# Optimization experiments

Measured on AMD Instinct MI355X. Metric: run time of the kernel, lower is better.

## Reference

```python
import jax, jax.numpy as jnp
import numpy as np

THRESHOLD = 0.5
MARGIN = 0.5
MIN_PIXELS = 64


def make_grid(h, w):
    # Faithful to SpatialClustering.make_grid
    if w >= h:
        xm = jnp.broadcast_to(jnp.linspace(0.0, w / h, w).reshape(1, 1, w), (1, h, w))
        ym = jnp.broadcast_to(jnp.linspace(0.0, 1.0, h).reshape(1, h, 1), (1, h, w))
    else:
        xm = jnp.broadcast_to(jnp.linspace(0.0, 1.0, w).reshape(1, 1, w), (1, h, w))
        ym = jnp.broadcast_to(jnp.linspace(0.0, h / w, h).reshape(1, h, 1), (1, h, w))
    return jnp.concatenate([xm, ym], axis=0)  # (2, h, w)


def cluster_per_image(x, grid_flat):
    # x: (5, h, w); grid_flat: (2, N)
    c, h, w = x.shape
    N = h * w
    offset = x[0:2].reshape(2, N)
    sigma = x[2:4].reshape(2, N)
    seed_raw = x[4].reshape(N)

    spa_emb = jnp.tanh(offset) + grid_flat          # (2, N)
    seed_map = jax.nn.sigmoid(seed_raw)             # (N,)
    valid = seed_raw > THRESHOLD                    # (N,) == torch `mask`

    # In torch: masked_select restricts to `valid` pixels; here we keep the
    # full N-length arrays and carry `valid`/`unclustered` boolean masks.
    # unclustered starts as `valid`, so the torch outer guard
    # (mask.sum() > min_pixels) coincides with the first while-cond check.

    def cond(state):
        unclustered, inst, count, done = state
        return (jnp.sum(unclustered) > MIN_PIXELS) & jnp.logical_not(done)

    def body(state):
        unclustered, inst, count, done = state
        score = jnp.where(unclustered, seed_map, 0.0)
        idx = jnp.argmax(score)
        sc = score[idx]
        new_done = sc < THRESHOLD  # torch `break` -> revert this iteration's updates

        uncl2 = unclustered.at[idx].set(False)  # torch: unclustered[seed] = 0 before ratio
        center = spa_emb[:, idx]                # (2,)
        s = sigma[:, idx]                       # (2,)
        # exp(-sum((e-c)^2 / (2 s^2)))
        dist = jnp.exp(-jnp.sum((spa_emb - center[:, None]) ** 2 / (2.0 * s[:, None] ** 2), axis=0))  # (N,)
        proposal = (dist > MARGIN) & valid

        pc = jnp.sum(proposal)
        uc = jnp.sum(proposal & uncl2)
        # torch: proposal.sum() > min_pixels  and  unclustered[proposal].sum()/proposal.sum() > 0.5
        accept = (pc > MIN_PIXELS) & (2 * uc > pc)

        inst_new = jnp.where(accept & proposal, count, inst)
        count_new = count + accept.astype(jnp.int32)
        uncl_new = uncl2 & jnp.logical_not(proposal)  # torch: unclustered[proposal] = 0

        unclustered = jnp.where(new_done, unclustered, uncl_new)
        inst = jnp.where(new_done, inst, inst_new)
        count = jnp.where(new_done, count, count_new)
        return (unclustered, inst, count, new_done)

    init = (valid, jnp.zeros(N, dtype=jnp.int32), jnp.int32(1), jnp.array(False))
    _, inst, _, _ = jax.lax.while_loop(cond, body, init)
    return inst.reshape(h, w)


def setup_inputs() -> dict:
    key = jax.random.key(0)
    k1, k2, k3 = jax.random.split(key, 3)
    B, H, W = 4, 512, 1024
    offset = jax.random.normal(k1, (B, 2, H, W), dtype=jnp.float32)
    # sigma in [0.2, 0.45]: realistic per-pixel bandwidths so exp-distance
    # proposals cover cluster-sized regions and the greedy loop terminates.
    sigma = jax.random.uniform(k2, (B, 2, H, W), dtype=jnp.float32, minval=0.2, maxval=0.45)
    seed = jax.random.normal(k3, (B, 1, H, W), dtype=jnp.float32)
    tag_pred = jnp.concatenate([offset, sigma, seed], axis=1)  # (B, 5, H, W)
    return {"tag_pred": tag_pred}


def reference(tag_pred):
    b, c, h, w = tag_pred.shape
    grid_flat = make_grid(h, w).reshape(2, h * w)
    f = lambda x: cluster_per_image(x, grid_flat)
    inst = jax.lax.map(f, tag_pred)  # sequential per-image greedy clustering
    return inst.astype(jnp.uint8)    # (b, h, w) instance map, ids 0 = background
```

## Files before the change

kernel.cpp:

```cpp
#include <hip/hip_runtime.h>
#include <math.h>

#define BATCH 4
#define HH 512
#define WW 1024
#define NPIX (HH*WW)
#define CCAP 196608
#define GX 64
#define GY 48
#define NCELL (GX*GY)
#define CELL 0.0625f
#define INVCELL 16.0f
#define SEGSZ 512
#define NSEGMAX (CCAP/SEGSZ)
#define DLCAP 2048
#define CKCAP 800
#define CKBCAP 512

__device__ __forceinline__ float xla_tanhf(float x) {
  if (fabsf(x) < 0.0004f) return x;
  float xc = fminf(fmaxf(x, -7.90531110763549805f), 7.90531110763549805f);
  float x2 = __fmul_rn(xc, xc);
  float p = -2.76076847742355e-16f;
  p = fmaf(x2, p, 2.00018790482477e-13f);
  p = fmaf(x2, p, -8.60467152213735e-11f);
  p = fmaf(x2, p, 5.12229709037114e-08f);
  p = fmaf(x2, p, 1.48572235717979e-05f);
  p = fmaf(x2, p, 6.37261928875436e-04f);
  p = fmaf(x2, p, 4.89352455891786e-03f);
  p = __fmul_rn(xc, p);
  float q = fmaf(x2, 1.19825839466702e-06f, 1.18534705686654e-04f);
  q = fmaf(x2, q, 2.26843463243900e-03f);
  q = fmaf(x2, q, 4.89352518554385e-03f);
  return __fdiv_rn(p, q);
}

__device__ __forceinline__ float xla_expf(float x) {
  float xc = fminf(fmaxf(x, -87.3365478515625f), 88.72283935546875f);
  float m = floorf(fmaf(xc, 1.44269504088896341f, 0.5f));
  float r = fmaf(m, -0.693359375f, xc);
  r = fmaf(m, 2.12194440e-4f, r);
  float r2 = __fmul_rn(r, r);
  float p = 1.9875691500e-4f;
  p = fmaf(p, r, 1.3981999507e-3f);
  p = fmaf(p, r, 8.3334519073e-3f);
  p = fmaf(p, r, 4.1665795894e-2f);
  p = fmaf(p, r, 1.6666665459e-1f);
  p = fmaf(p, r, 5.0000001201e-1f);
  float y = fmaf(r2, p, r);
  y = __fadd_rn(y, 1.0f);
  return ldexpf(y, (int)m);
}

__device__ __forceinline__ float xla_sigmoidf(float x) {
  return fmaf(0.5f, xla_tanhf(__fmul_rn(0.5f, x)), 0.5f);
}

__device__ __forceinline__ bool prop_test(float2 e, float cx, float cy,
                                          float den0, float den1,
                                          float inv0, float inv1) {
  float d0 = __fsub_rn(e.x, cx), d1 = __fsub_rn(e.y, cy);
  float dd0 = __fmul_rn(d0, d0), dd1 = __fmul_rn(d1, d1);
  float zf = fmaf(dd0, inv0, __fmul_rn(dd1, inv1));
  if (zf < 0.6921472f) return true;
  if (zf <= 0.6941472f) {
    float t0 = __fdiv_rn(dd0, den0);
    float t1 = __fdiv_rn(dd1, den1);
    float z = __fadd_rn(t0, t1);
    return xla_expf(-z) > 0.5f;
  }
  return false;
}

__device__ __forceinline__ int cell_of_x(float ex) {
  int c = (int)((ex + 1.0f) * INVCELL);
  return min(max(c, 0), GX - 1);
}
__device__ __forceinline__ int cell_of_y(float ey) {
  int c = (int)((ey + 1.0f) * INVCELL);
  return min(max(c, 0), GY - 1);
}

__device__ __forceinline__ unsigned wave_max_bcast_u32(unsigned x) {
  unsigned t;
  t = (unsigned)__builtin_amdgcn_update_dpp(0, (int)x, 0x111, 0xf, 0xf, false); if (t > x) x = t;
  t = (unsigned)__builtin_amdgcn_update_dpp(0, (int)x, 0x112, 0xf, 0xf, false); if (t > x) x = t;
  t = (unsigned)__builtin_amdgcn_update_dpp(0, (int)x, 0x114, 0xf, 0xf, false); if (t > x) x = t;
  t = (unsigned)__builtin_amdgcn_update_dpp(0, (int)x, 0x118, 0xf, 0xf, false); if (t > x) x = t;
  t = (unsigned)__builtin_amdgcn_update_dpp(0, (int)x, 0x142, 0xa, 0xf, false); if (t > x) x = t;
  t = (unsigned)__builtin_amdgcn_update_dpp(0, (int)x, 0x143, 0xc, 0xf, false); if (t > x) x = t;
  return (unsigned)__builtin_amdgcn_readlane((int)x, 63);
}

__device__ __forceinline__ int wave_sum_bcast_i32(int x) {
  x += __builtin_amdgcn_update_dpp(0, x, 0x111, 0xf, 0xf, false);
  x += __builtin_amdgcn_update_dpp(0, x, 0x112, 0xf, 0xf, false);
  x += __builtin_amdgcn_update_dpp(0, x, 0x114, 0xf, 0xf, false);
  x += __builtin_amdgcn_update_dpp(0, x, 0x118, 0xf, 0xf, false);
  x += __builtin_amdgcn_update_dpp(0, x, 0x142, 0xa, 0xf, false);
  x += __builtin_amdgcn_update_dpp(0, x, 0x143, 0xc, 0xf, false);
  return __builtin_amdgcn_readlane(x, 63);
}

__device__ __forceinline__ int wave_scan_incl_i32(int x) {
  x += __builtin_amdgcn_update_dpp(0, x, 0x111, 0xf, 0xf, false);
  x += __builtin_amdgcn_update_dpp(0, x, 0x112, 0xf, 0xf, false);
  x += __builtin_amdgcn_update_dpp(0, x, 0x114, 0xf, 0xf, false);
  x += __builtin_amdgcn_update_dpp(0, x, 0x118, 0xf, 0xf, false);
  x += __builtin_amdgcn_update_dpp(0, x, 0x142, 0xa, 0xf, false);
  x += __builtin_amdgcn_update_dpp(0, x, 0x143, 0xc, 0xf, false);
  return x;
}


__global__ __launch_bounds__(1024) void fill_kernel(int* out, int val, int n) {
  int i = blockIdx.x * 1024 + threadIdx.x;
  if (i < n) out[i] = val;
}

__global__ __launch_bounds__(1024) void hist_kernel(const float* __restrict__ in,
                                                    int* __restrict__ out,
                                                    int* __restrict__ hist) {
  __shared__ int lh[NCELL];
  int tid = threadIdx.x;
  int gid = blockIdx.x * 1024 + tid;
  int b = gid >> 19;
  int p = gid & (NPIX - 1);
  for (int j = tid; j < NCELL; j += 1024) lh[j] = 0;
  __syncthreads();
  const float* base = in + (size_t)b * 5 * NPIX;
  float seed = base[(size_t)4 * NPIX + p];
  out[gid] = 0;
  if (seed > 0.5f) {
    float ox = base[p];
    float oy = base[(size_t)NPIX + p];
    int col = p & (WW - 1);
    int row = p >> 10;
    float gx = __fmul_rn((float)col, 2.0f / 1023.0f);
    float gy = __fmul_rn((float)row, 1.0f / 511.0f);
    float ex = __fadd_rn(xla_tanhf(ox), gx);
    float ey = __fadd_rn(xla_tanhf(oy), gy);
    atomicAdd(&lh[cell_of_y(ey) * GX + cell_of_x(ex)], 1);
  }
  __syncthreads();
  for (int j = tid; j < NCELL; j += 1024) {
    int c = lh[j];
    if (c) atomicAdd(&hist[b * NCELL + j], c);
  }
}

__global__ __launch_bounds__(1024) void scan_kernel(const int* __restrict__ hist,
                                                    int* __restrict__ off,
                                                    int* __restrict__ cursor) {
  __shared__ int s_c[NCELL];
  __shared__ int s_ps[1024];
  int b = blockIdx.x, t = threadIdx.x;
  const int* h = hist + b * NCELL;
  for (int i = t; i < NCELL; i += 1024) s_c[i] = h[i];
  __syncthreads();
  int a = s_c[3 * t], b2 = s_c[3 * t + 1], c2 = s_c[3 * t + 2];
  int th = a + b2 + c2;
  s_ps[t] = th;
  __syncthreads();
  for (int d = 1; d < 1024; d <<= 1) {
    int v = (t >= d) ? s_ps[t - d] : 0;
    __syncthreads();
    s_ps[t] += v;
    __syncthreads();
  }
  int excl = s_ps[t] - th;
  int* ob = off + b * (NCELL + 1);
  int* cb = cursor + b * NCELL;
  ob[3 * t] = excl;              cb[3 * t] = excl;
  ob[3 * t + 1] = excl + a;      cb[3 * t + 1] = excl + a;
  ob[3 * t + 2] = excl + a + b2; cb[3 * t + 2] = excl + a + b2;
  if (t == 1023) ob[NCELL] = s_ps[1023];
}

__global__ __launch_bounds__(1024) void scatter_kernel(const float* __restrict__ in,
                                                       int* __restrict__ cursor,
                                                       float2* __restrict__ emb,
                                                       int2* __restrict__ pk) {
  __shared__ int lh[NCELL];
  __shared__ int lbase[NCELL];
  int tid = threadIdx.x;
  int gid = blockIdx.x * 1024 + tid;
  int b = gid >> 19;
  int p = gid & (NPIX - 1);
  for (int j = tid; j < NCELL; j += 1024) lh[j] = 0;
  __syncthreads();
  const float* base = in + (size_t)b * 5 * NPIX;
  float seed = base[(size_t)4 * NPIX + p];
  bool valid = seed > 0.5f;
  float ex = 0.0f, ey = 0.0f, smv = 0.0f;
  int cell = 0, sl = 0;
  if (valid) {
    float ox = base[p];
    float oy = base[(size_t)NPIX + p];
    int col = p & (WW - 1);
    int row = p >> 10;
    float gx = __fmul_rn((float)col, 2.0f / 1023.0f);
    float gy = __fmul_rn((float)row, 1.0f / 511.0f);
    ex = __fadd_rn(xla_tanhf(ox), gx);
    ey = __fadd_rn(xla_tanhf(oy), gy);
    smv = xla_sigmoidf(seed);
    cell = cell_of_y(ey) * GX + cell_of_x(ex);
    sl = atomicAdd(&lh[cell], 1);
  }
  __syncthreads();
  for (int j = tid; j < NCELL; j += 1024) {
    int c = lh[j];
    if (c) lbase[j] = atomicAdd(&cursor[b * NCELL + j], c);
  }
  __syncthreads();
  if (valid) {
    int slot = lbase[cell] + sl;
    if (slot < CCAP) {
      emb[(size_t)b * CCAP + slot] = make_float2(ex, ey);
      pk[(size_t)b * CCAP + slot]  = make_int2(__float_as_int(smv), p);
    }
  }
}

__device__ __forceinline__ void seg_rescan(int s, int V, int lane,
    const unsigned* s_uncl, const int2* __restrict__ pk,
    const float2* __restrict__ emb, const float* __restrict__ base,
    unsigned long long* s_segkey, int* s_segci, float4* s_segaux,
    float4* s_segaux2, bool checkAlive) {
  unsigned long long bk = 0ULL; int bci = -1; int bpx = 0;
  #pragma unroll
  for (int j = 0; j < 8; ++j) {
    int i = (s << 9) + (j << 6) + lane;
    if (i < V) {
      bool alive = !checkAlive || ((s_uncl[i >> 5] >> (i & 31)) & 1u);
      if (alive) {
        int2 v = pk[i];
        unsigned long long k = ((unsigned long long)(unsigned)v.x << 32) | (unsigned)(~v.y);
        if (k > bk) { bk = k; bci = i; bpx = v.y; }
      }
    }
  }
  unsigned bs = (unsigned)(bk >> 32);
  unsigned ms = wave_max_bcast_u32(bs);
  if (ms == 0u) {
    if (lane == 0) { s_segkey[s] = 0ULL; s_segci[s] = -1; }
    return;
  }
  unsigned long long tie = __ballot(bs == ms);
  bool winner;
  if (__popcll(tie) == 1ULL) {
    winner = (bs == ms);
  } else {
    unsigned long long mk = bk;
    #pragma unroll
    for (int o = 1; o < 64; o <<= 1) {
      unsigned long long ok = __shfl_xor(mk, o);
      if (ok > mk) mk = ok;
    }
    winner = (bk == mk);
  }
  if (winner) {
    s_segkey[s] = bk; s_segci[s] = bci;
    float2 e = emb[bci];
    float sxv = base[(size_t)2 * NPIX + bpx];
    float syv = base[(size_t)3 * NPIX + bpx];
    float d0 = __fmul_rn(2.0f, __fmul_rn(sxv, sxv));
    float d1 = __fmul_rn(2.0f, __fmul_rn(syv, syv));
    s_segaux[s] = make_float4(e.x, e.y, d0, d1);
    float i0v = 1.0f / d0;
    float i1v = 1.0f / d1;
    float ryv = sqrtf(__fmul_rn(d1, 0.6971472f)) * 1.00001f;
    s_segaux2[s] = make_float4(i0v, i1v, ryv, 0.0f);
  }
}

__global__ __launch_bounds__(1024) void cluster_kernel(const float* __restrict__ in,
                                                       int* __restrict__ out,
                                                       const float2* __restrict__ emb_all,
                                                       const int2* __restrict__ pk_all,
                                                       const int* __restrict__ off_g) {
  __shared__ unsigned int s_uncl[CCAP / 32];
  __shared__ int s_off[NCELL + 1];
  __shared__ unsigned long long s_segkey[NSEGMAX];
  __shared__ int s_segci[NSEGMAX];
  __shared__ float4 s_segaux[NSEGMAX];
  __shared__ float4 s_segaux2[NSEGMAX];
  __shared__ int s_dlist[DLCAP];
  __shared__ unsigned long long s_ck[CKCAP];
  __shared__ ulonglong2 s_ckbA[CKBCAP];
  __shared__ ulonglong2 s_ckbB[CKBCAP];
  __shared__ int s_pc[2];
  __shared__ int s_uc[2];
  __shared__ int s_nd[2];

  int b = blockIdx.x;
  int tid = threadIdx.x;
  int lane = tid & 63;
  int wid = tid >> 6;
  const int* offb = off_g + b * (NCELL + 1);
  int V = offb[NCELL];
  const float2* emb = emb_all + (size_t)b * CCAP;
  const int2*   pk  = pk_all  + (size_t)b * CCAP;
  int* outb = out + (size_t)b * NPIX;
  const float* base = in + (size_t)b * 5 * NPIX;

  if (V > CCAP) {
    for (int i = tid; i < NPIX; i += 1024) outb[i] = 1000000;
    return;
  }
  int NSEG = (V + SEGSZ - 1) >> 9;
  int Vm1 = V - 1;

  for (int i = tid; i <= NCELL; i += 1024) s_off[i] = offb[i];
  for (int w = tid; w < CCAP / 32; w += 1024) {
    int basebit = w << 5;
    unsigned m;
    if (basebit + 32 <= V)      m = 0xffffffffu;
    else if (basebit >= V)      m = 0u;
    else                        m = (1u << (V - basebit)) - 1u;
    s_uncl[w] = m;
  }
  if (tid < 2) { s_pc[tid] = 0; s_uc[tid] = 0; s_nd[tid] = 0; }
  __syncthreads();

  for (int s = wid; s < NSEG; s += 16)
    seg_rescan(s, V, lane, s_uncl, pk, emb, base, s_segkey, s_segci, s_segaux,
               s_segaux2, false);
  __syncthreads();

  int ucount = V, count = 1, guard = 0;
  int t = 0;
  while (ucount > 64 && guard++ <= CCAP) {
    int cur = t & 1, nxt = cur ^ 1;

    unsigned long long lk = 0ULL; int lsg = -1;
    for (int s = lane; s < NSEG; s += 64) {
      unsigned long long v = s_segkey[s];
      if (v > lk) { lk = v; lsg = s; }
    }
    unsigned ls = (unsigned)(lk >> 32);
    unsigned gs = wave_max_bcast_u32(ls);
    if (gs == 0u) break;
    float sm = __uint_as_float(gs);
    if (sm < 0.5f) break;
    unsigned long long bmask = __ballot(ls == gs);
    int src, sg;
    if (__popcll(bmask) == 1ULL) {
      src = __builtin_ctzll(bmask);
      sg = __shfl(lsg, src);
    } else {
      unsigned long long gk = lk;
      #pragma unroll
      for (int o = 1; o < 64; o <<= 1) {
        unsigned long long ok = __shfl_xor(gk, o);
        if (ok > gk) gk = ok;
      }
      unsigned long long bm2 = __ballot(lk == gk);
      src = __builtin_ctzll(bm2);
      sg = __shfl(lsg, src);
    }

    float4 aux = s_segaux[sg];
    float4 ax2 = s_segaux2[sg];
    float cx = aux.x, cy = aux.y, den0 = aux.z, den1 = aux.w;
    float inv0 = ax2.x;
    float inv1 = ax2.y;
    float ry = ax2.z;
    int r0 = cell_of_y(cy - ry);
    int r1 = cell_of_y(cy + ry);
    int nr = r1 - r0 + 1;

    int ck = 0, rs_l = 0, re_l = 0, m0_l = 0, m1_l = 0, startl = 0;
    if (lane < nr) {
      int r = r0 + lane;
      float ylo = fmaf((float)r, CELL, -1.0f);
      float dy = fmaxf(0.0f, fmaxf(ylo - cy, cy - (ylo + CELL))) * 0.999999f;
      float rem = 0.6971472f - dy * dy * inv1;
      if (rem > 0.0f) {
        float dxm = sqrtf(den0 * rem) * 1.00001f;
        int c0 = cell_of_x(cx - dxm), c1 = cell_of_x(cx + dxm);
        int rbase = r * GX;
        rs_l = s_off[rbase + c0]; re_l = s_off[rbase + c1 + 1];
        m0_l = rs_l; m1_l = rs_l;
        float dyc = fmaxf(fabsf(ylo - cy), fabsf(ylo + CELL - cy)) + 1e-5f;
        float remI = 0.6920f - dyc * dyc * inv1;
        if (remI > 0.0f) {
          float dxin = sqrtf(den0 * remI) * 0.9999f;
          int a  = (int)ceilf(fmaf(cx - dxin, INVCELL, INVCELL) + 1e-3f);
          int bb = (int)floorf(fmaf(cx + dxin, INVCELL, INVCELL) - 1e-3f) - 1;
          a = max(a, c0); bb = min(bb, c1);
          if (a <= bb) { m0_l = s_off[rbase + a]; m1_l = s_off[rbase + bb + 1]; }
        }
        startl = rs_l & ~31;
        ck = (re_l > rs_l) ? ((re_l - startl + 255) >> 8) : 0;
      }
    }
    int cum = wave_scan_incl_i32(ck);
    int nc = __builtin_amdgcn_readlane(cum, 63);
    int excl = cum - ck;
    if (lane < nr && ck) {
      for (int k = 0; k < ck; ++k) {
        int i0k = startl + (k << 8);
        int ssk = max(rs_l - i0k, 0);
        int lok = min(max(m0_l - i0k, 0), 256);
        int h2k = min(max(m1_l - i0k, 0), 256);
        int enk = min(re_l - i0k, 256);
        s_ck[excl + k] = (unsigned long long)(unsigned)(i0k >> 5)
                       | ((unsigned long long)(unsigned)ssk << 13)
                       | ((unsigned long long)(unsigned)lok << 19)
                       | ((unsigned long long)(unsigned)h2k << 28)
                       | ((unsigned long long)(unsigned)enk << 37);
      }
    }

    int pc = 0, uc = 0;
    int c = wid;
    unsigned long long ed = (c < nc) ? s_ck[c] : 0ULL;
    while (c < nc) {
      int cn = c + 16;
      unsigned long long epre = (cn < nc) ? s_ck[cn] : 0ULL;
      int i0 = ((int)(ed & 0x1fff)) << 5;
      int ss = (int)((ed >> 13) & 0x3f);
      int lo = (int)((ed >> 19) & 0x1ff);
      int h2 = (int)((ed >> 28) & 0x1ff);
      int en = (int)((ed >> 37) & 0x1ff);
      int idx1 = lane + 64, idx2 = lane + 128, idx3 = lane + 192;
      bool p0, p1, p2, p3;
      if (lo <= ss && h2 >= en) {
        p0 = lane >= ss && lane < en;
        p1 = idx1 < en; p2 = idx2 < en; p3 = idx3 < en;
      } else {
        int ia = min(i0 + lane, Vm1),  ib = min(i0 + idx1, Vm1);
        int ic = min(i0 + idx2, Vm1),  id = min(i0 + idx3, Vm1);
        float2 e0 = emb[ia], e1 = emb[ib], e2 = emb[ic], e3 = emb[id];
        bool t0 = prop_test(e0, cx, cy, den0, den1, inv0, inv1);
        bool t1 = prop_test(e1, cx, cy, den0, den1, inv0, inv1);
        bool t2 = prop_test(e2, cx, cy, den0, den1, inv0, inv1);
        bool t3 = prop_test(e3, cx, cy, den0, den1, inv0, inv1);
        p0 = (lane >= ss && lane < en) && ((lane >= lo && lane < h2) || t0);
        p1 = (idx1 < en) && ((idx1 >= lo && idx1 < h2) || t1);
        p2 = (idx2 < en) && ((idx2 >= lo && idx2 < h2) || t2);
        p3 = (idx3 < en) && ((idx3 >= lo && idx3 < h2) || t3);
      }
      unsigned long long bm0 = __ballot(p0);
      unsigned long long bm1 = __ballot(p1);
      unsigned long long bm2 = __ballot(p2);
      unsigned long long bm3 = __ballot(p3);
      if (c < CKBCAP) {
        if (lane == 0)      { ulonglong2 v; v.x = bm0; v.y = bm1; s_ckbA[c] = v; }
        else if (lane == 1) { ulonglong2 v; v.x = bm2; v.y = bm3; s_ckbB[c] = v; }
      }
      if ((bm0 | bm1 | bm2 | bm3) != 0ULL && lane < 8) {
        unsigned long long bsel = (lane < 2) ? bm0 : (lane < 4) ? bm1
                                 : (lane < 6) ? bm2 : bm3;
        unsigned bits = (unsigned)(bsel >> ((lane & 1) << 5));
        pc += __popc(bits);
        if (bits) {
          unsigned tw = (unsigned)(i0 >> 5) + (unsigned)lane;
          unsigned old = atomicAnd(&s_uncl[tw], ~bits);
          unsigned remv = old & bits;
          if (remv) {
            uc += __popc(remv);
            int seg = (int)(tw >> 4);
            int ciw = s_segci[seg];
            if ((ciw >> 5) == (int)tw && ((remv >> (ciw & 31)) & 1u)) {
              int pos = atomicAdd(&s_nd[cur], 1);
              if (pos < DLCAP) s_dlist[pos] = seg;
            }
          }
        }
      }
      c = cn; ed = epre;
    }
    int pcW = wave_sum_bcast_i32(pc);
    int ucW = wave_sum_bcast_i32(uc);
    if (lane == 0 && (pcW | ucW)) {
      if (pcW) atomicAdd(&s_pc[cur], pcW);
      if (ucW) atomicAdd(&s_uc[cur], ucW);
    }
    __syncthreads();

    int pcT = s_pc[cur];
    int ucR = s_uc[cur];
    int ndRaw = s_nd[cur];
    bool accept = (pcT > 64) && (2 * (ucR - 1) > pcT);
    int label = count & 255;
    if (accept) count++;
    ucount -= ucR;
    if (tid == 0) { s_pc[nxt] = 0; s_uc[nxt] = 0; s_nd[nxt] = 0; }

    if (accept) {
      for (int c2 = wid; c2 < nc; c2 += 16) {
        unsigned long long e = s_ck[c2];
        int i0 = ((int)(e & 0x1fff)) << 5;
        if (c2 < CKBCAP) {
          ulonglong2 ba = s_ckbA[c2];
          ulonglong2 bb = s_ckbB[c2];
          if ((ba.x >> lane) & 1ULL) outb[pk[i0 + lane].y] = label;
          if ((ba.y >> lane) & 1ULL) outb[pk[i0 + 64 + lane].y] = label;
          if ((bb.x >> lane) & 1ULL) outb[pk[i0 + 128 + lane].y] = label;
          if ((bb.y >> lane) & 1ULL) outb[pk[i0 + 192 + lane].y] = label;
        } else {
          int ss = (int)((e >> 13) & 0x3f);
          int lo = (int)((e >> 19) & 0x1ff);
          int h2 = (int)((e >> 28) & 0x1ff);
          int en = (int)((e >> 37) & 0x1ff);
          #pragma unroll
          for (int g = 0; g < 4; ++g) {
            int idx = (g << 6) + lane;
            if (idx >= ss && idx < en &&
                ((idx >= lo && idx < h2) ||
                 prop_test(emb[i0 + idx], cx, cy, den0, den1, inv0, inv1)))
              outb[pk[i0 + idx].y] = label;
          }
        }
      }
    }

    if (ndRaw > DLCAP) {
      for (int s = wid; s < NSEG; s += 16)
        seg_rescan(s, V, lane, s_uncl, pk, emb, base, s_segkey, s_segci,
                   s_segaux, s_segaux2, true);
    } else {
      for (int d = wid; d < ndRaw; d += 16)
        seg_rescan(s_dlist[d], V, lane, s_uncl, pk, emb, base, s_segkey,
                   s_segci, s_segaux, s_segaux2, true);
    }
    __syncthreads();
    t++;
  }
}


extern "C" void kernel_launch(void* const* d_in, const int* in_sizes, int n_in,
                              void* d_out, int out_size, void* d_ws, size_t ws_size,
                              hipStream_t stream) {
  const float* in = (const float*)d_in[0];
  int* out = (int*)d_out;

  size_t hist_bytes = (size_t)BATCH * NCELL * sizeof(int);
  size_t off_bytes  = (size_t)BATCH * (NCELL + 1) * sizeof(int);
  size_t cur_bytes  = (size_t)BATCH * NCELL * sizeof(int);
  size_t emb_bytes  = (size_t)BATCH * CCAP * sizeof(float2);
  size_t pk_bytes   = (size_t)BATCH * CCAP * sizeof(int2);

  size_t o_hist = 256;
  size_t o_off  = (o_hist + hist_bytes + 255) & ~(size_t)255;
  size_t o_cur  = (o_off + off_bytes + 255) & ~(size_t)255;
  size_t o_emb  = (o_cur + cur_bytes + 255) & ~(size_t)255;
  size_t o_pk   = (o_emb + emb_bytes + 255) & ~(size_t)255;
  size_t need   = o_pk + pk_bytes;

  if (ws_size < need) {
    fill_kernel<<<(out_size + 1023) / 1024, 1024, 0, stream>>>(out, 2000000, out_size);
    return;
  }

  int*    hist = (int*)((char*)d_ws + o_hist);
  int*    off  = (int*)((char*)d_ws + o_off);
  int*    cur  = (int*)((char*)d_ws + o_cur);
  float2* emb  = (float2*)((char*)d_ws + o_emb);
  int2*   pk   = (int2*)((char*)d_ws + o_pk);

  hipMemsetAsync(hist, 0, hist_bytes, stream);
  hist_kernel<<<(BATCH * NPIX) / 1024, 1024, 0, stream>>>(in, out, hist);
  scan_kernel<<<BATCH, 1024, 0, stream>>>(hist, off, cur);
  scatter_kernel<<<(BATCH * NPIX) / 1024, 1024, 0, stream>>>(in, cur, emb, pk);
  cluster_kernel<<<BATCH, 1024, 0, stream>>>(in, out, emb, pk, off);
}
```

Measured before the change: 796.5 us.

## Process two non-overlapping seeds per greedy iteration with per-wave dynamic chunk scheduling

```diff
diff --git a/kernel.cpp b/kernel.cpp
--- a/kernel.cpp
+++ b/kernel.cpp
@@ -14,7 +14,8 @@
 #define SEGSZ 512
 #define NSEGMAX (CCAP/SEGSZ)
 #define DLCAP 2048
-#define CKCAP 800
+#define CKSEED 800
+#define CKCAP (2*CKSEED)
 #define CKBCAP 512
 
 __device__ __forceinline__ float xla_tanhf(float x) {
@@ -81,17 +82,6 @@
   return min(max(c, 0), GY - 1);
 }
 
-__device__ __forceinline__ unsigned wave_max_bcast_u32(unsigned x) {
-  unsigned t;
-  t = (unsigned)__builtin_amdgcn_update_dpp(0, (int)x, 0x111, 0xf, 0xf, false); if (t > x) x = t;
-  t = (unsigned)__builtin_amdgcn_update_dpp(0, (int)x, 0x112, 0xf, 0xf, false); if (t > x) x = t;
-  t = (unsigned)__builtin_amdgcn_update_dpp(0, (int)x, 0x114, 0xf, 0xf, false); if (t > x) x = t;
-  t = (unsigned)__builtin_amdgcn_update_dpp(0, (int)x, 0x118, 0xf, 0xf, false); if (t > x) x = t;
-  t = (unsigned)__builtin_amdgcn_update_dpp(0, (int)x, 0x142, 0xa, 0xf, false); if (t > x) x = t;
-  t = (unsigned)__builtin_amdgcn_update_dpp(0, (int)x, 0x143, 0xc, 0xf, false); if (t > x) x = t;
-  return (unsigned)__builtin_amdgcn_readlane((int)x, 63);
-}
-
 __device__ __forceinline__ int wave_sum_bcast_i32(int x) {
   x += __builtin_amdgcn_update_dpp(0, x, 0x111, 0xf, 0xf, false);
   x += __builtin_amdgcn_update_dpp(0, x, 0x112, 0xf, 0xf, false);
@@ -110,6 +100,18 @@
   x += __builtin_amdgcn_update_dpp(0, x, 0x142, 0xa, 0xf, false);
   x += __builtin_amdgcn_update_dpp(0, x, 0x143, 0xc, 0xf, false);
   return x;
+}
+
+__device__ __forceinline__ void wave_max_key64(unsigned &h, unsigned &l) {
+#define KSTEP(ctrl, rm)                                                        \
+  { unsigned nh = (unsigned)__builtin_amdgcn_update_dpp(0, (int)h, ctrl, rm, 0xf, false); \
+    unsigned nl = (unsigned)__builtin_amdgcn_update_dpp(0, (int)l, ctrl, rm, 0xf, false); \
+    if (nh > h || (nh == h && nl > l)) { h = nh; l = nl; } }
+  KSTEP(0x111, 0xf) KSTEP(0x112, 0xf) KSTEP(0x114, 0xf) KSTEP(0x118, 0xf)
+  KSTEP(0x142, 0xa) KSTEP(0x143, 0xc)
+#undef KSTEP
+  h = (unsigned)__builtin_amdgcn_readlane((int)h, 63);
+  l = (unsigned)__builtin_amdgcn_readlane((int)l, 63);
 }
 
 
@@ -225,9 +227,9 @@
 __device__ __forceinline__ void seg_rescan(int s, int V, int lane,
     const unsigned* s_uncl, const int2* __restrict__ pk,
     const float2* __restrict__ emb, const float* __restrict__ base,
-    unsigned long long* s_segkey, int* s_segci, float4* s_segaux,
-    float4* s_segaux2, bool checkAlive) {
-  unsigned long long bk = 0ULL; int bci = -1; int bpx = 0;
+    unsigned long long* s_segkey, unsigned long long* s_segkey2,
+    int* s_segci, float4* s_segaux, float4* s_segaux2, bool checkAlive) {
+  unsigned k1h = 0, k1l = 0, k2h = 0, k2l = 0; int ci1 = -1, bpx = 0;
   #pragma unroll
   for (int j = 0; j < 8; ++j) {
     int i = (s << 9) + (j << 6) + lane;
@@ -235,33 +237,30 @@
       bool alive = !checkAlive || ((s_uncl[i >> 5] >> (i & 31)) & 1u);
       if (alive) {
         int2 v = pk[i];
-        unsigned long long k = ((unsigned long long)(unsigned)v.x << 32) | (unsigned)(~v.y);
-        if (k > bk) { bk = k; bci = i; bpx = v.y; }
-      }
-    }
-  }
-  unsigned bs = (unsigned)(bk >> 32);
-  unsigned ms = wave_max_bcast_u32(bs);
-  if (ms == 0u) {
-    if (lane == 0) { s_segkey[s] = 0ULL; s_segci[s] = -1; }
+        unsigned vh = (unsigned)v.x, vl = (unsigned)(~v.y);
+        if (vh > k1h || (vh == k1h && vl > k1l)) {
+          k2h = k1h; k2l = k1l; k1h = vh; k1l = vl; ci1 = i; bpx = v.y;
+        } else if (vh > k2h || (vh == k2h && vl > k2l)) {
+          k2h = vh; k2l = vl;
+        }
+      }
+    }
+  }
+  unsigned m1h = k1h, m1l = k1l;
+  wave_max_key64(m1h, m1l);
+  if (m1h == 0u) {
+    if (lane == 0) { s_segkey[s] = 0ULL; s_segkey2[s] = 0ULL; s_segci[s] = -1; }
     return;
   }
-  unsigned long long tie = __ballot(bs == ms);
-  bool winner;
-  if (__popcll(tie) == 1ULL) {
-    winner = (bs == ms);
-  } else {
-    unsigned long long mk = bk;
-    #pragma unroll
-    for (int o = 1; o < 64; o <<= 1) {
-      unsigned long long ok = __shfl_xor(mk, o);
-      if (ok > mk) mk = ok;
-    }
-    winner = (bk == mk);
-  }
-  if (winner) {
-    s_segkey[s] = bk; s_segci[s] = bci;
-    float2 e = emb[bci];
+  bool own = (k1h == m1h && k1l == m1l);
+  unsigned ch = own ? k2h : k1h, cl = own ? k2l : k1l;
+  unsigned m2h = ch, m2l = cl;
+  wave_max_key64(m2h, m2l);
+  if (lane == 0) s_segkey2[s] = ((unsigned long long)m2h << 32) | m2l;
+  if (own) {
+    s_segkey[s] = ((unsigned long long)m1h << 32) | m1l;
+    s_segci[s] = ci1;
+    float2 e = emb[ci1];
     float sxv = base[(size_t)2 * NPIX + bpx];
     float syv = base[(size_t)3 * NPIX + bpx];
     float d0 = __fmul_rn(2.0f, __fmul_rn(sxv, sxv));
@@ -270,7 +269,8 @@
     float i0v = 1.0f / d0;
     float i1v = 1.0f / d1;
     float ryv = sqrtf(__fmul_rn(d1, 0.6971472f)) * 1.00001f;
-    s_segaux2[s] = make_float4(i0v, i1v, ryv, 0.0f);
+    float rxv = sqrtf(__fmul_rn(d0, 0.6971472f)) * 1.00001f;
+    s_segaux2[s] = make_float4(i0v, i1v, ryv, rxv);
   }
 }
 
@@ -282,16 +282,19 @@
   __shared__ unsigned int s_uncl[CCAP / 32];
   __shared__ int s_off[NCELL + 1];
   __shared__ unsigned long long s_segkey[NSEGMAX];
+  __shared__ unsigned long long s_segkey2[NSEGMAX];
   __shared__ int s_segci[NSEGMAX];
   __shared__ float4 s_segaux[NSEGMAX];
   __shared__ float4 s_segaux2[NSEGMAX];
   __shared__ int s_dlist[DLCAP];
   __shared__ unsigned long long s_ck[CKCAP];
-  __shared__ ulonglong2 s_ckbA[CKBCAP];
-  __shared__ ulonglong2 s_ckbB[CKBCAP];
-  __shared__ int s_pc[2];
-  __shared__ int s_uc[2];
+  __shared__ ulonglong2 s_ckbA[2 * CKBCAP];
+  __shared__ ulonglong2 s_ckbB[2 * CKBCAP];
+  __shared__ int s_pc4[4];
+  __shared__ int s_uc4[4];
+  __shared__ int s_ckpos4[4];
   __shared__ int s_nd[2];
+  __shared__ int s_ncq[2];
 
   int b = blockIdx.x;
   int tid = threadIdx.x;
@@ -320,12 +323,13 @@
     else                        m = (1u << (V - basebit)) - 1u;
     s_uncl[w] = m;
   }
-  if (tid < 2) { s_pc[tid] = 0; s_uc[tid] = 0; s_nd[tid] = 0; }
+  if (tid < 4) { s_pc4[tid] = 0; s_uc4[tid] = 0; s_ckpos4[tid] = 0; }
+  if (tid < 2) { s_nd[tid] = 0; }
   __syncthreads();
 
   for (int s = wid; s < NSEG; s += 16)
-    seg_rescan(s, V, lane, s_uncl, pk, emb, base, s_segkey, s_segci, s_segaux,
-               s_segaux2, false);
+    seg_rescan(s, V, lane, s_uncl, pk, emb, base, s_segkey, s_segkey2,
+               s_segci, s_segaux, s_segaux2, false);
   __syncthreads();
 
   int ucount = V, count = 1, guard = 0;
@@ -333,61 +337,80 @@
   while (ucount > 64 && guard++ <= CCAP) {
     int cur = t & 1, nxt = cur ^ 1;
 
-    unsigned long long lk = 0ULL; int lsg = -1;
+    unsigned a1h = 0, a1l = 0, a2h = 0, a2l = 0; int asg1 = -1, asg2 = -1;
     for (int s = lane; s < NSEG; s += 64) {
       unsigned long long v = s_segkey[s];
-      if (v > lk) { lk = v; lsg = s; }
-    }
-    unsigned ls = (unsigned)(lk >> 32);
-    unsigned gs = wave_max_bcast_u32(ls);
-    if (gs == 0u) break;
-    float sm = __uint_as_float(gs);
-    if (sm < 0.5f) break;
-    unsigned long long bmask = __ballot(ls == gs);
-    int src, sg;
-    if (__popcll(bmask) == 1ULL) {
-      src = __builtin_ctzll(bmask);
-      sg = __shfl(lsg, src);
-    } else {
-      unsigned long long gk = lk;
-      #pragma unroll
-      for (int o = 1; o < 64; o <<= 1) {
-        unsigned long long ok = __shfl_xor(gk, o);
-        if (ok > gk) gk = ok;
-      }
-      unsigned long long bm2 = __ballot(lk == gk);
-      src = __builtin_ctzll(bm2);
-      sg = __shfl(lsg, src);
-    }
-
-    float4 aux = s_segaux[sg];
-    float4 ax2 = s_segaux2[sg];
-    float cx = aux.x, cy = aux.y, den0 = aux.z, den1 = aux.w;
-    float inv0 = ax2.x;
-    float inv1 = ax2.y;
-    float ry = ax2.z;
-    int r0 = cell_of_y(cy - ry);
-    int r1 = cell_of_y(cy + ry);
+      unsigned vh = (unsigned)(v >> 32), vl = (unsigned)v;
+      if (vh > a1h || (vh == a1h && vl > a1l)) {
+        a2h = a1h; a2l = a1l; asg2 = asg1; a1h = vh; a1l = vl; asg1 = s;
+      } else if (vh > a2h || (vh == a2h && vl > a2l)) {
+        a2h = vh; a2l = vl; asg2 = s;
+      }
+    }
+    unsigned m1h = a1h, m1l = a1l;
+    wave_max_key64(m1h, m1l);
+    if (m1h == 0u) break;
+    if (__uint_as_float(m1h) < 0.5f) break;
+    bool own1 = (a1h == m1h && a1l == m1l);
+    int src1 = __builtin_ctzll(__ballot(own1));
+    int sg1 = __shfl(asg1, src1);
+    unsigned ch = own1 ? a2h : a1h, cl2 = own1 ? a2l : a1l;
+    int csg = own1 ? asg2 : asg1;
+    unsigned m2h = ch, m2l = cl2;
+    wave_max_key64(m2h, m2l);
+
+    float4 auxA = s_segaux[sg1];
+    float4 ax2A = s_segaux2[sg1];
+    int kk = 1, sg2 = -1;
+    float4 auxB = make_float4(0.f, 0.f, 1.f, 1.f);
+    float4 ax2B = make_float4(1.f, 1.f, 0.f, 0.f);
+    if (m2h != 0u) {
+      bool own2 = (ch == m2h && cl2 == m2l);
+      int src2 = __builtin_ctzll(__ballot(own2));
+      sg2 = __shfl(csg, src2);
+      unsigned long long k2s = s_segkey2[sg1];
+      unsigned kh = (unsigned)(k2s >> 32), kl = (unsigned)k2s;
+      bool hidden_bigger = (kh > m2h) || (kh == m2h && kl > m2l);
+      if (!hidden_bigger) {
+        auxB = s_segaux[sg2];
+        ax2B = s_segaux2[sg2];
+        bool ovl = (fabsf(auxA.x - auxB.x) <= (ax2A.w + ax2B.w)) &&
+                   (fabsf(auxA.y - auxB.y) <= (ax2A.z + ax2B.z));
+        if (!ovl) kk = 2;
+      }
+    }
+
+    int myseed = (kk == 2) ? (wid & 1) : 0;
+    float cxS = myseed ? auxB.x : auxA.x;
+    float cyS = myseed ? auxB.y : auxA.y;
+    float d0S = myseed ? auxB.z : auxA.z;
+    float d1S = myseed ? auxB.w : auxA.w;
+    float i0S = myseed ? ax2B.x : ax2A.x;
+    float i1S = myseed ? ax2B.y : ax2A.y;
+    float ryS = myseed ? ax2B.z : ax2A.z;
+    int qb = myseed * CKSEED;
+    int r0 = cell_of_y(cyS - ryS);
+    int r1 = cell_of_y(cyS + ryS);
     int nr = r1 - r0 + 1;
 
     int ck = 0, rs_l = 0, re_l = 0, m0_l = 0, m1_l = 0, startl = 0;
     if (lane < nr) {
       int r = r0 + lane;
       float ylo = fmaf((float)r, CELL, -1.0f);
-      float dy = fmaxf(0.0f, fmaxf(ylo - cy, cy - (ylo + CELL))) * 0.999999f;
-      float rem = 0.6971472f - dy * dy * inv1;
+      float dy = fmaxf(0.0f, fmaxf(ylo - cyS, cyS - (ylo + CELL))) * 0.999999f;
+      float rem = 0.6971472f - dy * dy * i1S;
       if (rem > 0.0f) {
-        float dxm = sqrtf(den0 * rem) * 1.00001f;
-        int c0 = cell_of_x(cx - dxm), c1 = cell_of_x(cx + dxm);
+        float dxm = sqrtf(d0S * rem) * 1.00001f;
+        int c0 = cell_of_x(cxS - dxm), c1 = cell_of_x(cxS + dxm);
         int rbase = r * GX;
         rs_l = s_off[rbase + c0]; re_l = s_off[rbase + c1 + 1];
         m0_l = rs_l; m1_l = rs_l;
-        float dyc = fmaxf(fabsf(ylo - cy), fabsf(ylo + CELL - cy)) + 1e-5f;
-        float remI = 0.6920f - dyc * dyc * inv1;
+        float dyc = fmaxf(fabsf(ylo - cyS), fabsf(ylo + CELL - cyS)) + 1e-5f;
+        float remI = 0.6920f - dyc * dyc * i1S;
         if (remI > 0.0f) {
-          float dxin = sqrtf(den0 * remI) * 0.9999f;
-          int a  = (int)ceilf(fmaf(cx - dxin, INVCELL, INVCELL) + 1e-3f);
-          int bb = (int)floorf(fmaf(cx + dxin, INVCELL, INVCELL) - 1e-3f) - 1;
+          float dxin = sqrtf(d0S * remI) * 0.9999f;
+          int a  = (int)ceilf(fmaf(cxS - dxin, INVCELL, INVCELL) + 1e-3f);
+          int bb = (int)floorf(fmaf(cxS + dxin, INVCELL, INVCELL) - 1e-3f) - 1;
           a = max(a, c0); bb = min(bb, c1);
           if (a <= bb) { m0_l = s_off[rbase + a]; m1_l = s_off[rbase + bb + 1]; }
         }
@@ -396,29 +419,35 @@
       }
     }
     int cum = wave_scan_incl_i32(ck);
-    int nc = __builtin_amdgcn_readlane(cum, 63);
+    int ncmine = __builtin_amdgcn_readlane(cum, 63);
     int excl = cum - ck;
+    if (ncmine > CKSEED) ncmine = CKSEED;
     if (lane < nr && ck) {
       for (int k = 0; k < ck; ++k) {
+        int q = excl + k;
+        if (q >= CKSEED) break;
         int i0k = startl + (k << 8);
         int ssk = max(rs_l - i0k, 0);
         int lok = min(max(m0_l - i0k, 0), 256);
         int h2k = min(max(m1_l - i0k, 0), 256);
         int enk = min(re_l - i0k, 256);
-        s_ck[excl + k] = (unsigned long long)(unsigned)(i0k >> 5)
-                       | ((unsigned long long)(unsigned)ssk << 13)
-                       | ((unsigned long long)(unsigned)lok << 19)
-                       | ((unsigned long long)(unsigned)h2k << 28)
-                       | ((unsigned long long)(unsigned)enk << 37);
-      }
-    }
+        s_ck[qb + q] = (unsigned long long)(unsigned)(i0k >> 5)
+                     | ((unsigned long long)(unsigned)ssk << 13)
+                     | ((unsigned long long)(unsigned)lok << 19)
+                     | ((unsigned long long)(unsigned)h2k << 28)
+                     | ((unsigned long long)(unsigned)enk << 37);
+      }
+    }
+    if (lane == 0) s_ncq[myseed] = ncmine;
 
     int pc = 0, uc = 0;
-    int c = wid;
-    unsigned long long ed = (c < nc) ? s_ck[c] : 0ULL;
-    while (c < nc) {
-      int cn = c + 16;
-      unsigned long long epre = (cn < nc) ? s_ck[cn] : 0ULL;
+    int* ckposp = &s_ckpos4[cur * 2 + myseed];
+    for (;;) {
+      int pos;
+      if (lane == 0) pos = atomicAdd(ckposp, 1);
+      pos = __shfl(pos, 0);
+      if (pos >= ncmine) break;
+      unsigned long long ed = s_ck[qb + pos];
       int i0 = ((int)(ed & 0x1fff)) << 5;
       int ss = (int)((ed >> 13) & 0x3f);
       int lo = (int)((ed >> 19) & 0x1ff);
@@ -433,10 +462,10 @@
         int ia = min(i0 + lane, Vm1),  ib = min(i0 + idx1, Vm1);
         int ic = min(i0 + idx2, Vm1),  id = min(i0 + idx3, Vm1);
         float2 e0 = emb[ia], e1 = emb[ib], e2 = emb[ic], e3 = emb[id];
-        bool t0 = prop_test(e0, cx, cy, den0, den1, inv0, inv1);
-        bool t1 = prop_test(e1, cx, cy, den0, den1, inv0, inv1);
-        bool t2 = prop_test(e2, cx, cy, den0, den1, inv0, inv1);
-        bool t3 = prop_test(e3, cx, cy, den0, den1, inv0, inv1);
+        bool t0 = prop_test(e0, cxS, cyS, d0S, d1S, i0S, i1S);
+        bool t1 = prop_test(e1, cxS, cyS, d0S, d1S, i0S, i1S);
+        bool t2 = prop_test(e2, cxS, cyS, d0S, d1S, i0S, i1S);
+        bool t3 = prop_test(e3, cxS, cyS, d0S, d1S, i0S, i1S);
         p0 = (lane >= ss && lane < en) && ((lane >= lo && lane < h2) || t0);
         p1 = (idx1 < en) && ((idx1 >= lo && idx1 < h2) || t1);
         p2 = (idx2 < en) && ((idx2 >= lo && idx2 < h2) || t2);
@@ -446,9 +475,10 @@
       unsigned long long bm1 = __ballot(p1);
       unsigned long long bm2 = __ballot(p2);
       unsigned long long bm3 = __ballot(p3);
-      if (c < CKBCAP) {
-        if (lane == 0)      { ulonglong2 v; v.x = bm0; v.y = bm1; s_ckbA[c] = v; }
-        else if (lane == 1) { ulonglong2 v; v.x = bm2; v.y = bm3; s_ckbB[c] = v; }
+      if (pos < CKBCAP) {
+        int bidx = (myseed << 9) + pos;
+        if (lane == 0)      { ulonglong2 v; v.x = bm0; v.y = bm1; s_ckbA[bidx] = v; }
+        else if (lane == 1) { ulonglong2 v; v.x = bm2; v.y = bm3; s_ckbB[bidx] = v; }
       }
       if ((bm0 | bm1 | bm2 | bm3) != 0ULL && lane < 8) {
         unsigned long long bsel = (lane < 2) ? bm0 : (lane < 4) ? bm1
@@ -464,42 +494,51 @@
             int seg = (int)(tw >> 4);
             int ciw = s_segci[seg];
             if ((ciw >> 5) == (int)tw && ((remv >> (ciw & 31)) & 1u)) {
-              int pos = atomicAdd(&s_nd[cur], 1);
-              if (pos < DLCAP) s_dlist[pos] = seg;
+              int dpos = atomicAdd(&s_nd[cur], 1);
+              if (dpos < DLCAP) s_dlist[dpos] = seg;
             }
           }
         }
       }
-      c = cn; ed = epre;
     }
     int pcW = wave_sum_bcast_i32(pc);
     int ucW = wave_sum_bcast_i32(uc);
     if (lane == 0 && (pcW | ucW)) {
-      if (pcW) atomicAdd(&s_pc[cur], pcW);
-      if (ucW) atomicAdd(&s_uc[cur], ucW);
+      if (pcW) atomicAdd(&s_pc4[cur * 2 + myseed], pcW);
+      if (ucW) atomicAdd(&s_uc4[cur * 2 + myseed], ucW);
     }
     __syncthreads();
 
-    int pcT = s_pc[cur];
-    int ucR = s_uc[cur];
+    int pcT0 = s_pc4[cur * 2 + 0], ucR0 = s_uc4[cur * 2 + 0];
+    int pcT1 = s_pc4[cur * 2 + 1], ucR1 = s_uc4[cur * 2 + 1];
     int ndRaw = s_nd[cur];
-    bool accept = (pcT > 64) && (2 * (ucR - 1) > pcT);
-    int label = count & 255;
-    if (accept) count++;
-    ucount -= ucR;
-    if (tid == 0) { s_pc[nxt] = 0; s_uc[nxt] = 0; s_nd[nxt] = 0; }
-
-    if (accept) {
-      for (int c2 = wid; c2 < nc; c2 += 16) {
+    int nc0 = s_ncq[0];
+    int nc1q = (kk == 2) ? s_ncq[1] : 0;
+    bool acc0 = (pcT0 > 64) && (2 * (ucR0 - 1) > pcT0);
+    bool valid1 = (kk == 2) && (ucount - ucR0 > 64);
+    bool acc1 = valid1 && (pcT1 > 64) && (2 * (ucR1 - 1) > pcT1);
+    int label0 = count & 255; if (acc0) count++;
+    int label1 = count & 255; if (acc1) count++;
+    ucount -= ucR0;
+    if (valid1) ucount -= ucR1;
+    if (tid == 0) {
+      s_pc4[nxt * 2] = 0; s_pc4[nxt * 2 + 1] = 0;
+      s_uc4[nxt * 2] = 0; s_uc4[nxt * 2 + 1] = 0;
+      s_nd[nxt] = 0;
+      s_ckpos4[nxt * 2] = 0; s_ckpos4[nxt * 2 + 1] = 0;
+    }
+
+    if (acc0) {
+      for (int c2 = wid; c2 < nc0; c2 += 16) {
         unsigned long long e = s_ck[c2];
         int i0 = ((int)(e & 0x1fff)) << 5;
         if (c2 < CKBCAP) {
           ulonglong2 ba = s_ckbA[c2];
           ulonglong2 bb = s_ckbB[c2];
-          if ((ba.x >> lane) & 1ULL) outb[pk[i0 + lane].y] = label;
-          if ((ba.y >> lane) & 1ULL) outb[pk[i0 + 64 + lane].y] = label;
-          if ((bb.x >> lane) & 1ULL) outb[pk[i0 + 128 + lane].y] = label;
-          if ((bb.y >> lane) & 1ULL) outb[pk[i0 + 192 + lane].y] = label;
+          if ((ba.x >> lane) & 1ULL) outb[pk[i0 + lane].y] = label0;
+          if ((ba.y >> lane) & 1ULL) outb[pk[i0 + 64 + lane].y] = label0;
+          if ((bb.x >> lane) & 1ULL) outb[pk[i0 + 128 + lane].y] = label0;
+          if ((bb.y >> lane) & 1ULL) outb[pk[i0 + 192 + lane].y] = label0;
         } else {
           int ss = (int)((e >> 13) & 0x3f);
           int lo = (int)((e >> 19) & 0x1ff);
@@ -510,21 +549,52 @@
             int idx = (g << 6) + lane;
             if (idx >= ss && idx < en &&
                 ((idx >= lo && idx < h2) ||
-                 prop_test(emb[i0 + idx], cx, cy, den0, den1, inv0, inv1)))
-              outb[pk[i0 + idx].y] = label;
+                 prop_test(emb[i0 + idx], auxA.x, auxA.y, auxA.z, auxA.w,
+                           ax2A.x, ax2A.y)))
+              outb[pk[i0 + idx].y] = label0;
           }
         }
       }
     }
+    if (acc1) {
+      for (int c2 = wid; c2 < nc1q; c2 += 16) {
+        unsigned long long e = s_ck[CKSEED + c2];
+        int i0 = ((int)(e & 0x1fff)) << 5;
+        if (c2 < CKBCAP) {
+          ulonglong2 ba = s_ckbA[CKBCAP + c2];
+          ulonglong2 bb = s_ckbB[CKBCAP + c2];
+          if ((ba.x >> lane) & 1ULL) outb[pk[i0 + lane].y] = label1;
+          if ((ba.y >> lane) & 1ULL) outb[pk[i0 + 64 + lane].y] = label1;
+          if ((bb.x >> lane) & 1ULL) outb[pk[i0 + 128 + lane].y] = label1;
+          if ((bb.y >> lane) & 1ULL) outb[pk[i0 + 192 + lane].y] = label1;
+        } else {
+          int ss = (int)((e >> 13) & 0x3f);
+          int lo = (int)((e >> 19) & 0x1ff);
+          int h2 = (int)((e >> 28) & 0x1ff);
+          int en = (int)((e >> 37) & 0x1ff);
+          #pragma unroll
+          for (int g = 0; g < 4; ++g) {
+            int idx = (g << 6) + lane;
+            if (idx >= ss && idx < en &&
+                ((idx >= lo && idx < h2) ||
+                 prop_test(emb[i0 + idx], auxB.x, auxB.y, auxB.z, auxB.w,
+                           ax2B.x, ax2B.y)))
+              outb[pk[i0 + idx].y] = label1;
+          }
+        }
+      }
+    }
+
+    if (kk == 2 && !valid1) break;
 
     if (ndRaw > DLCAP) {
       for (int s = wid; s < NSEG; s += 16)
-        seg_rescan(s, V, lane, s_uncl, pk, emb, base, s_segkey, s_segci,
-                   s_segaux, s_segaux2, true);
+        seg_rescan(s, V, lane, s_uncl, pk, emb, base, s_segkey, s_segkey2,
+                   s_segci, s_segaux, s_segaux2, true);
     } else {
       for (int d = wid; d < ndRaw; d += 16)
         seg_rescan(s_dlist[d], V, lane, s_uncl, pk, emb, base, s_segkey,
-                   s_segci, s_segaux, s_segaux2, true);
+                   s_segkey2, s_segci, s_segaux, s_segaux2, true);
     }
     __syncthreads();
     t++;
```

Result: slower. 822.0 us (+3.2%).
